# Kernel tuning notes

Measured on AMD Instinct MI355X. Metric: run time of the kernel, lower is better.

The kernel has to match this reference:

```python
import jax, jax.numpy as jnp
import numpy as np

N = 50000
E = 800000
D = 128          # feature_dimension
H = 2 * D        # hidden = 2*feature_dimension
C = 8            # num_edge_colours


def setup_inputs() -> dict:
    key = jax.random.key(0)
    ks = jax.random.split(key, 9)
    x = jax.random.normal(ks[0], (N, D), dtype=jnp.float32)
    edge_index = jax.random.randint(ks[1], (2, E), 0, N, dtype=jnp.int64)
    edge_colour = jax.random.randint(ks[2], (E,), 0, C, dtype=jnp.int64)
    # conv weights init: normal(0, 0.001) as in the torch module
    W_conv1 = 0.001 * jax.random.normal(ks[3], (C, H, D), dtype=jnp.float32)
    W_conv2 = 0.001 * jax.random.normal(ks[4], (C, D, H), dtype=jnp.float32)
    # nn.Linear default init: U(-1/sqrt(fan_in), 1/sqrt(fan_in))
    b1 = 1.0 / np.sqrt(D)
    b2 = 1.0 / np.sqrt(H)
    W_self1 = jax.random.uniform(ks[5], (H, D), jnp.float32, -b1, b1)
    b_self1 = jax.random.uniform(ks[6], (H,), jnp.float32, -b1, b1)
    W_self2 = jax.random.uniform(ks[7], (D, H), jnp.float32, -b2, b2)
    b_self2 = jax.random.uniform(ks[8], (D,), jnp.float32, -b2, b2)
    return {
        "x": x, "edge_index": edge_index, "edge_colour": edge_colour,
        "W_self1": W_self1, "b_self1": b_self1,
        "W_self2": W_self2, "b_self2": b_self2,
        "W_conv1": W_conv1, "W_conv2": W_conv2,
    }


def _ec_conv(h, src, seg, Wc):
    # Per-colour gather -> scatter-add -> colour-specific linear, summed over colours.
    # seg = colour * N + dst combines (colour, dst) into one segment id so a single
    # segment_sum covers all colours (equivalent to the per-colour masked loops).
    msgs = h[src]                                             # [E, F]
    agg = jax.ops.segment_sum(msgs, seg, num_segments=C * N)  # [C*N, F]
    agg = agg.reshape(C, N, h.shape[1])                       # [C, N, F]
    return jnp.einsum('cnf,cof->no', agg, Wc)                 # [N, O]


def reference(x, edge_index, edge_colour, W_self1, b_self1, W_self2, b_self2,
              W_conv1, W_conv2):
    src = edge_index[0]   # message() uses x_j = x[src], aggregated at dst
    dst = edge_index[1]
    seg = edge_colour * N + dst
    h = x @ W_self1.T + b_self1 + _ec_conv(x, src, seg, W_conv1)
    h = jax.nn.relu(h)
    h2 = h @ W_self2.T + b_self2 + _ec_conv(h, src, seg, W_conv2)
    return jax.nn.sigmoid(h2 - 10.0)
```

## Files before the change

### kernel.cpp

```cpp
#include <hip/hip_runtime.h>


#define NN 50000
#define EE 800000
#define DD 128
#define HH 256
#define CC 8
#define K1 1152

typedef unsigned short u16;
typedef __attribute__((ext_vector_type(8))) short s16x8;
typedef __attribute__((ext_vector_type(4))) float f32x4;

__device__ __forceinline__ float bf2f(short u) {
  return __uint_as_float(((unsigned)(u16)u) << 16);
}
__device__ __forceinline__ u16 f2bf(float f) {
  unsigned u = __float_as_uint(f);
  u = (u + 0x7FFFu + ((u >> 16) & 1u)) >> 16;
  return (u16)u;
}


__global__ void k_castx(const float* __restrict__ x, u16* __restrict__ xb) {
  int i = blockIdx.x * 256 + threadIdx.x;
  if (i < NN * DD) xb[i] = f2bf(x[i]);
}

__global__ void k_wt1f(const float* __restrict__ Wc1, const float* __restrict__ Ws1,
                       u16* __restrict__ W) {
  int i = blockIdx.x * 256 + threadIdx.x;
  if (i >= 294912) return;
  int e = i & 7;
  int t = i >> 3;
  int rs = t & 15; t >>= 4;
  int kg = t & 3;  t >>= 2;
  int kk = t % 36;
  int col16 = t / 36;
  int col = col16 * 16 + rs;
  int k = kk * 32 + kg * 8 + e;
  float v = (k < CC * DD) ? Wc1[(k >> 7) * (HH * DD) + col * DD + (k & 127)]
                          : Ws1[col * DD + (k - CC * DD)];
  W[i] = f2bf(v);
}

__global__ void k_wt2f(const float* __restrict__ Wc2, const float* __restrict__ Ws2,
                       u16* __restrict__ W) {
  int i = blockIdx.x * 256 + threadIdx.x;
  if (i >= 294912) return;
  int e = i & 7;
  int t = i >> 3;
  int rs = t & 15; t >>= 4;
  int kg = t & 3;  t >>= 2;
  int kk = t & 7;
  int col16 = t >> 3;
  int oc = col16 * 16 + rs;
  int c = oc >> 7, o = oc & 127;
  int k = kk * 32 + kg * 8 + e;
  float v = (c < CC) ? Wc2[c * (DD * HH) + o * HH + k] : Ws2[o * HH + k];
  W[i] = f2bf(v);
}


__global__ void k_hist(const int* __restrict__ ei, const int* __restrict__ ec,
                       int* __restrict__ counts) {
  int e = blockIdx.x * 256 + threadIdx.x;
  if (e < EE) {
    int dst = ei[EE + e];
    int c = ec[e];
    atomicAdd(&counts[dst * CC + c], 1);
  }
}

__global__ void k_offsets(const int* __restrict__ counts, int2* __restrict__ oc,
                          int* __restrict__ cursor, int* __restrict__ gcount) {
  __shared__ int lds[256];
  __shared__ int basesh;
  int tid = threadIdx.x;
  int i = blockIdx.x * 256 + tid;
  int c = (i < CC * NN) ? counts[i] : 0;
  lds[tid] = c;
  __syncthreads();
  int v = c;
  for (int s = 1; s < 256; s <<= 1) {
    int t = (tid >= s) ? lds[tid - s] : 0;
    __syncthreads();
    v += t;
    lds[tid] = v;
    __syncthreads();
  }
  if (tid == 255) basesh = atomicAdd(gcount, v);
  __syncthreads();
  int excl = basesh + v - c;
  if (i < CC * NN) {
    oc[i] = make_int2(excl, c);
    cursor[i] = excl;
  }
}

__global__ void k_fill(const int* __restrict__ ei, const int* __restrict__ ec,
                       int* __restrict__ cursor, int* __restrict__ sv) {
  int e = blockIdx.x * 256 + threadIdx.x;
  if (e < EE) {
    int src = ei[e];
    int dst = ei[EE + e];
    int c = ec[e];
    int slot = atomicAdd(&cursor[dst * CC + c], 1);
    sv[slot] = src * 8 + c;
  }
}


__global__ void __launch_bounds__(256) k_agg1(
    const u16* __restrict__ xb, const int2* __restrict__ oc,
    const int* __restrict__ sv, u16* __restrict__ agg) {
  int item = blockIdx.x * 256 + threadIdx.x;
  int dst = item >> 4, ch = item & 15;
  int eoff = ch * 8;
#pragma unroll
  for (int c = 0; c < CC; ++c) {
    int2 se = oc[dst * CC + c];
    float s[8];
#pragma unroll
    for (int q = 0; q < 8; q++) s[q] = 0.f;
    int j = 0;
    for (; j + 1 < se.y; j += 2) {
      int s0 = sv[se.x + j] >> 3;
      int s1 = sv[se.x + j + 1] >> 3;
      s16x8 v0 = *(const s16x8*)(xb + (size_t)s0 * DD + eoff);
      s16x8 v1 = *(const s16x8*)(xb + (size_t)s1 * DD + eoff);
#pragma unroll
      for (int q = 0; q < 8; q++) s[q] += bf2f(v0[q]) + bf2f(v1[q]);
    }
    if (j < se.y) {
      int s0 = sv[se.x + j] >> 3;
      s16x8 v0 = *(const s16x8*)(xb + (size_t)s0 * DD + eoff);
#pragma unroll
      for (int q = 0; q < 8; q++) s[q] += bf2f(v0[q]);
    }
    s16x8 r;
#pragma unroll
    for (int q = 0; q < 8; q++) r[q] = (short)f2bf(s[q]);
    *(s16x8*)(agg + ((size_t)c * NN + dst) * DD + eoff) = r;
  }
}


__global__ void __launch_bounds__(256, 2) k_gemm1s(
    const u16* __restrict__ xb, const u16* __restrict__ agg,
    const u16* __restrict__ Wf, const float* __restrict__ b1,
    u16* __restrict__ hb) {
  int tid = threadIdx.x;
  int w = tid >> 6, lane = tid & 63;
  int rs = lane & 15, kg = lane >> 4;
  int rt = w >> 1, ch = w & 1;
  int r0 = blockIdx.x * 128 + rt * 64;

  int rowA[4];
#pragma unroll
  for (int rg = 0; rg < 4; ++rg) rowA[rg] = min(r0 + rg * 16 + rs, NN - 1);

  f32x4 acc[4][8];
#pragma unroll
  for (int rg = 0; rg < 4; ++rg)
#pragma unroll
    for (int i = 0; i < 8; i++)
#pragma unroll
      for (int q = 0; q < 4; q++) acc[rg][i][q] = 0.f;

  for (int c = 0; c < CC; ++c) {
#pragma unroll
    for (int kk = 0; kk < 4; ++kk) {
      int kkg = c * 4 + kk;
      s16x8 af[4];
#pragma unroll
      for (int rg = 0; rg < 4; ++rg)
        af[rg] = *(const s16x8*)(agg + ((size_t)c * NN + rowA[rg]) * DD + kk * 32 + kg * 8);
#pragma unroll
      for (int fc = 0; fc < 8; ++fc) {
        int col16 = ch * 8 + fc;
        s16x8 bfr = *(const s16x8*)(Wf + (size_t)(col16 * 36 + kkg) * 512 + lane * 8);
#pragma unroll
        for (int rg = 0; rg < 4; ++rg)
          acc[rg][fc] = __builtin_amdgcn_mfma_f32_16x16x32_bf16(af[rg], bfr, acc[rg][fc], 0, 0, 0);
      }
    }
  }
#pragma unroll
  for (int kk = 0; kk < 4; ++kk) {
    int kkg = 32 + kk;
    s16x8 af[4];
#pragma unroll
    for (int rg = 0; rg < 4; ++rg)
      af[rg] = *(const s16x8*)(xb + (size_t)rowA[rg] * DD + kk * 32 + kg * 8);
#pragma unroll
    for (int fc = 0; fc < 8; ++fc) {
      int col16 = ch * 8 + fc;
      s16x8 bfr = *(const s16x8*)(Wf + (size_t)(col16 * 36 + kkg) * 512 + lane * 8);
#pragma unroll
      for (int rg = 0; rg < 4; ++rg)
        acc[rg][fc] = __builtin_amdgcn_mfma_f32_16x16x32_bf16(af[rg], bfr, acc[rg][fc], 0, 0, 0);
    }
  }

#pragma unroll
  for (int fc = 0; fc < 8; ++fc) {
    int col = ch * 128 + fc * 16 + rs;
    float bias = b1[col];
#pragma unroll
    for (int rg = 0; rg < 4; ++rg) {
#pragma unroll
      for (int q = 0; q < 4; ++q) {
        float v = acc[rg][fc][q] + bias;
        if (v < 0.f) v = 0.f;
        int rr = r0 + rg * 16 + kg * 4 + q;
        if (rr < NN) hb[(size_t)rr * HH + col] = f2bf(v);
      }
    }
  }
}


__global__ void __launch_bounds__(256, 3) k_gemm2g(
    const u16* __restrict__ hb, const u16* __restrict__ Wf,
    u16* __restrict__ g2) {
  __shared__ u16 Bs[24576];
  int cb = blockIdx.x;
  int rb = blockIdx.y;
  int tid = threadIdx.x;
  int w = tid >> 6, lane = tid & 63;
  int rs = lane & 15, kg = lane >> 4;
  int c16b = cb * 6;

  {
    const u16* src = Wf + (size_t)cb * 24576;
#pragma unroll
    for (int i = 0; i < 12; ++i) {
      int o = (i * 256 + tid) * 8;
      *(s16x8*)(Bs + o) = *(const s16x8*)(src + o);
    }
  }
  __syncthreads();

#pragma unroll
  for (int tt = 0; tt < 2; ++tt) {
    int t = w + tt * 4;
    int r0 = rb * 256 + t * 32;
    int rowA[2];
#pragma unroll
    for (int rg = 0; rg < 2; ++rg) rowA[rg] = min(r0 + rg * 16 + rs, NN - 1);

    s16x8 af[2][8];
#pragma unroll
    for (int rg = 0; rg < 2; ++rg)
#pragma unroll
      for (int kk = 0; kk < 8; ++kk)
        af[rg][kk] = *(const s16x8*)(hb + (size_t)rowA[rg] * HH + kk * 32 + kg * 8);

    f32x4 acc[2][6];
#pragma unroll
    for (int rg = 0; rg < 2; ++rg)
#pragma unroll
      for (int i = 0; i < 6; i++)
#pragma unroll
        for (int q = 0; q < 4; q++) acc[rg][i][q] = 0.f;

#pragma unroll
    for (int kk = 0; kk < 8; ++kk) {
#pragma unroll
      for (int fc = 0; fc < 6; ++fc) {
        s16x8 bfr = *(const s16x8*)(Bs + ((fc * 8 + kk) * 64 + lane) * 8);
#pragma unroll
        for (int rg = 0; rg < 2; ++rg)
          acc[rg][fc] = __builtin_amdgcn_mfma_f32_16x16x32_bf16(af[rg][kk], bfr, acc[rg][fc], 0, 0, 0);
      }
    }

#pragma unroll
    for (int rg = 0; rg < 2; ++rg) {
#pragma unroll
      for (int q = 0; q < 4; ++q) {
        int rr = r0 + rg * 16 + kg * 4 + q;
        if (rr < NN) {
#pragma unroll
          for (int fc = 0; fc < 6; ++fc) {
            int col = (c16b + fc) * 16 + rs;
            g2[(size_t)rr * 1152 + col] = f2bf(acc[rg][fc][q]);
          }
        }
      }
    }
  }
}


__global__ void __launch_bounds__(256) k_final(
    const u16* __restrict__ g2, const float* __restrict__ b2,
    const int2* __restrict__ oc, const int* __restrict__ sv,
    float* __restrict__ out) {
  int item = blockIdx.x * 256 + threadIdx.x;
  if (item >= NN * 8) return;
  int dst = item >> 3, ch = item & 7;
  int eoff = ch * 16;

  int st, cn;
  {
    int2 a0 = oc[dst * CC];
    int2 a7 = oc[dst * CC + 7];
    st = a0.x;
    cn = a7.x + a7.y - a0.x;
  }

  float s[16];
  {
    const u16* sp = g2 + (size_t)dst * 1152 + 1024 + eoff;
    s16x8 lo = *(const s16x8*)sp;
    s16x8 hi = *(const s16x8*)(sp + 8);
#pragma unroll
    for (int q = 0; q < 8; q++) s[q] = b2[eoff + q] + bf2f(lo[q]);
#pragma unroll
    for (int q = 0; q < 8; q++) s[q + 8] = b2[eoff + 8 + q] + bf2f(hi[q]);
  }

  for (int j = 0; j < cn; j += 4) {
    int pofs[4];
#pragma unroll
    for (int t = 0; t < 4; t++) {
      int jj = j + t;
      if (jj < cn) {
        int v = sv[st + jj];
        pofs[t] = (v >> 3) * 1152 + (v & 7) * 128;
      } else {
        pofs[t] = -1;
      }
    }
#pragma unroll
    for (int t = 0; t < 4; t++) {
      if (pofs[t] >= 0) {
        const u16* pp = g2 + pofs[t] + eoff;
        s16x8 lo = *(const s16x8*)pp;
        s16x8 hi = *(const s16x8*)(pp + 8);
#pragma unroll
        for (int q = 0; q < 8; q++) s[q] += bf2f(lo[q]);
#pragma unroll
        for (int q = 0; q < 8; q++) s[q + 8] += bf2f(hi[q]);
      }
    }
  }
  float* op = out + (size_t)dst * DD + eoff;
#pragma unroll
  for (int q = 0; q < 16; q++) op[q] = 1.f / (1.f + expf(10.f - s[q]));
}


extern "C" void kernel_launch(void* const* d_in, const int* in_sizes, int n_in,
                              void* d_out, int out_size, void* d_ws, size_t ws_size,
                              hipStream_t stream) {
  const float* x   = (const float*)d_in[0];
  const int*   ei  = (const int*)d_in[1];
  const int*   ec  = (const int*)d_in[2];
  const float* Ws1 = (const float*)d_in[3];
  const float* b1  = (const float*)d_in[4];
  const float* Ws2 = (const float*)d_in[5];
  const float* b2  = (const float*)d_in[6];
  const float* Wc1 = (const float*)d_in[7];
  const float* Wc2 = (const float*)d_in[8];
  float* out = (float*)d_out;

  char* p = (char*)d_ws;
  u16*  g2     = (u16*)p;
  u16*  agg1   = (u16*)p;
  u16*  xb     = (u16*)(p + 102400000);
  u16*  hb     = (u16*)(p + 115200000);
  u16*  W1f    = (u16*)(p + 140800000);
  u16*  W2f    = (u16*)(p + 141389824);
  int2* oc     = (int2*)(p + 141979648);
  int*  sv     = (int*)(p + 145179648);
  int*  counts = (int*)(p + 148379648);
  int*  gcount = (int*)(p + 149979648);
  int*  cursor = (int*)(p + 149979904);

  hipMemsetAsync(counts, 0, 1600256, stream);

  k_castx<<<25000, 256, 0, stream>>>(x, xb);
  k_wt1f<<<1152, 256, 0, stream>>>(Wc1, Ws1, W1f);
  k_wt2f<<<1152, 256, 0, stream>>>(Wc2, Ws2, W2f);

  k_hist<<<3125, 256, 0, stream>>>(ei, ec, counts);
  k_offsets<<<1563, 256, 0, stream>>>(counts, oc, cursor, gcount);
  k_fill<<<3125, 256, 0, stream>>>(ei, ec, cursor, sv);

  k_agg1<<<3125, 256, 0, stream>>>(xb, oc, sv, agg1);
  k_gemm1s<<<391, 256, 0, stream>>>(xb, agg1, W1f, b1, hb);
  k_gemm2g<<<dim3(12, 196), 256, 0, stream>>>(hb, W2f, g2);
  k_final<<<1563, 256, 0, stream>>>(g2, b2, oc, sv, out);
}
```

Measured before the change: 350.5 us.

## Stage gemm1 weight tiles in LDS and split output columns across blocks

```diff
diff --git a/kernel.cpp b/kernel.cpp
--- a/kernel.cpp
+++ b/kernel.cpp
@@ -146,61 +146,68 @@
 }
 
 
-__global__ void __launch_bounds__(256, 2) k_gemm1s(
+__global__ void __launch_bounds__(256, 4) k_gemm1s(
     const u16* __restrict__ xb, const u16* __restrict__ agg,
     const u16* __restrict__ Wf, const float* __restrict__ b1,
     u16* __restrict__ hb) {
+  __shared__ u16 Bs[16384];
+  int ch = blockIdx.x;
+  int rb = blockIdx.y;
   int tid = threadIdx.x;
   int w = tid >> 6, lane = tid & 63;
   int rs = lane & 15, kg = lane >> 4;
-  int rt = w >> 1, ch = w & 1;
-  int r0 = blockIdx.x * 128 + rt * 64;
-
-  int rowA[4];
-#pragma unroll
-  for (int rg = 0; rg < 4; ++rg) rowA[rg] = min(r0 + rg * 16 + rs, NN - 1);
-
-  f32x4 acc[4][8];
-#pragma unroll
-  for (int rg = 0; rg < 4; ++rg)
+  int r0 = rb * 128 + w * 32;
+
+  int rowA[2];
+#pragma unroll
+  for (int rg = 0; rg < 2; ++rg) rowA[rg] = min(r0 + rg * 16 + rs, NN - 1);
+
+  f32x4 acc[2][8];
+#pragma unroll
+  for (int rg = 0; rg < 2; ++rg)
 #pragma unroll
     for (int i = 0; i < 8; i++)
 #pragma unroll
       for (int q = 0; q < 4; q++) acc[rg][i][q] = 0.f;
 
-  for (int c = 0; c < CC; ++c) {
+  for (int ph = 0; ph < 9; ++ph) {
+#pragma unroll
+    for (int i = 0; i < 8; ++i) {
+      int li = i * 256 + tid;
+      int fc = li >> 8;
+      int u = li & 255;
+      int kkl = u >> 6, j = u & 63;
+      *(s16x8*)(Bs + (fc * 4 + kkl) * 512 + j * 8) =
+          *(const s16x8*)(Wf + (size_t)((ch * 8 + fc) * 36 + ph * 4 + kkl) * 512 + j * 8);
+    }
+    __syncthreads();
+
+    s16x8 af[2][4];
+    if (ph < CC) {
+#pragma unroll
+      for (int rg = 0; rg < 2; ++rg)
+#pragma unroll
+        for (int kk = 0; kk < 4; ++kk)
+          af[rg][kk] = *(const s16x8*)(agg + ((size_t)ph * NN + rowA[rg]) * DD + kk * 32 + kg * 8);
+    } else {
+#pragma unroll
+      for (int rg = 0; rg < 2; ++rg)
+#pragma unroll
+        for (int kk = 0; kk < 4; ++kk)
+          af[rg][kk] = *(const s16x8*)(xb + (size_t)rowA[rg] * DD + kk * 32 + kg * 8);
+    }
+
 #pragma unroll
     for (int kk = 0; kk < 4; ++kk) {
-      int kkg = c * 4 + kk;
-      s16x8 af[4];
-#pragma unroll
-      for (int rg = 0; rg < 4; ++rg)
-        af[rg] = *(const s16x8*)(agg + ((size_t)c * NN + rowA[rg]) * DD + kk * 32 + kg * 8);
 #pragma unroll
       for (int fc = 0; fc < 8; ++fc) {
-        int col16 = ch * 8 + fc;
-        s16x8 bfr = *(const s16x8*)(Wf + (size_t)(col16 * 36 + kkg) * 512 + lane * 8);
-#pragma unroll
-        for (int rg = 0; rg < 4; ++rg)
-          acc[rg][fc] = __builtin_amdgcn_mfma_f32_16x16x32_bf16(af[rg], bfr, acc[rg][fc], 0, 0, 0);
-      }
-    }
-  }
-#pragma unroll
-  for (int kk = 0; kk < 4; ++kk) {
-    int kkg = 32 + kk;
-    s16x8 af[4];
-#pragma unroll
-    for (int rg = 0; rg < 4; ++rg)
-      af[rg] = *(const s16x8*)(xb + (size_t)rowA[rg] * DD + kk * 32 + kg * 8);
-#pragma unroll
-    for (int fc = 0; fc < 8; ++fc) {
-      int col16 = ch * 8 + fc;
-      s16x8 bfr = *(const s16x8*)(Wf + (size_t)(col16 * 36 + kkg) * 512 + lane * 8);
-#pragma unroll
-      for (int rg = 0; rg < 4; ++rg)
-        acc[rg][fc] = __builtin_amdgcn_mfma_f32_16x16x32_bf16(af[rg], bfr, acc[rg][fc], 0, 0, 0);
-    }
+        s16x8 bfr = *(const s16x8*)(Bs + (fc * 4 + kk) * 512 + lane * 8);
+#pragma unroll
+        for (int rg = 0; rg < 2; ++rg)
+          acc[rg][fc] = __builtin_amdgcn_mfma_f32_16x16x32_bf16(af[rg][kk], bfr, acc[rg][fc], 0, 0, 0);
+      }
+    }
+    __syncthreads();
   }
 
 #pragma unroll
@@ -208,7 +215,7 @@
     int col = ch * 128 + fc * 16 + rs;
     float bias = b1[col];
 #pragma unroll
-    for (int rg = 0; rg < 4; ++rg) {
+    for (int rg = 0; rg < 2; ++rg) {
 #pragma unroll
       for (int q = 0; q < 4; ++q) {
         float v = acc[rg][fc][q] + bias;
@@ -391,7 +398,7 @@
   k_fill<<<3125, 256, 0, stream>>>(ei, ec, cursor, sv);
 
   k_agg1<<<3125, 256, 0, stream>>>(xb, oc, sv, agg1);
-  k_gemm1s<<<391, 256, 0, stream>>>(xb, agg1, W1f, b1, hb);
+  k_gemm1s<<<dim3(2, 391), 256, 0, stream>>>(xb, agg1, W1f, b1, hb);
   k_gemm2g<<<dim3(12, 196), 256, 0, stream>>>(hb, W2f, g2);
   k_final<<<1563, 256, 0, stream>>>(g2, b2, oc, sv, out);
 }
```

Result: faster. 341.0 us (-2.7%).
